# Kernel tuning notes

Hardware: AMD Instinct MI355X
Metric: run time of the kernel (lower is better)

Reference implementation:

```python
import jax, jax.numpy as jnp
import numpy as np

NTOKEN, NINP, NHID, NLAYERS = 32000, 1024, 1024, 2
SEQ, BATCH = 128, 32


def setup_inputs() -> dict:
    key = jax.random.key(0)
    ks = jax.random.split(key, 6)
    initrange = 0.1
    tokens = jax.random.randint(ks[0], (SEQ, BATCH), 0, NTOKEN)
    h0 = jnp.zeros((NLAYERS, BATCH, NHID), jnp.float32)
    c0 = jnp.zeros((NLAYERS, BATCH, NHID), jnp.float32)
    emb_table = jax.random.uniform(ks[1], (NTOKEN, NINP), jnp.float32, -initrange, initrange)
    # nn.Linear(2H, 4H): weight [4H, 2H]; store transposed [2H, 4H] for x @ W
    lstm_W = jax.random.normal(ks[2], (NLAYERS, 2 * NHID, 4 * NHID), jnp.float32) * (1.0 / np.sqrt(2 * NHID))
    lstm_b = jax.random.normal(ks[3], (NLAYERS, 4 * NHID), jnp.float32) * 0.01
    dec_W = jax.random.uniform(ks[4], (NHID, NTOKEN), jnp.float32, -initrange, initrange)
    dec_b = jnp.zeros((NTOKEN,), jnp.float32)
    return {"tokens": tokens, "h0": h0, "c0": c0, "emb_table": emb_table,
            "lstm_W": lstm_W, "lstm_b": lstm_b, "dec_W": dec_W, "dec_b": dec_b}


def _lstm_scan(emb, h0, c0, lstm_W, lstm_b):
    def step(carry, x_t):  # x_t: [B, H]
        h, c = carry  # each [L, B, H]
        hs, cs = [], []
        inp = x_t
        for l in range(NLAYERS):
            gates = jnp.concatenate([inp, h[l]], axis=1) @ lstm_W[l] + lstm_b[l]  # [B, 4H]
            i, j, f, o = jnp.split(gates, 4, axis=1)
            c_new = c[l] * jax.nn.sigmoid(f) + jax.nn.sigmoid(i) * jnp.tanh(j)
            h_new = jnp.tanh(c_new) * jax.nn.sigmoid(o)
            hs.append(h_new)
            cs.append(c_new)
            inp = h_new
        return (jnp.stack(hs), jnp.stack(cs)), inp

    (h_last, c_last), outputs = jax.lax.scan(step, (h0, c0), emb)
    return outputs, h_last, c_last  # outputs: [S, B, H]


def reference(tokens, h0, c0, emb_table, lstm_W, lstm_b, dec_W, dec_b):
    emb = emb_table[tokens]  # [S, B, NINP]
    outputs, h_last, c_last = _lstm_scan(emb, h0, c0, lstm_W, lstm_b)
    decoded = outputs @ dec_W + dec_b  # [S, B, NTOKEN]
    return decoded, (h_last, c_last)
```

## Files before the change

### kernel.cpp

```cpp
#include <hip/hip_runtime.h>

typedef __attribute__((ext_vector_type(8))) short bf16x8;
typedef __attribute__((ext_vector_type(4))) float f32x4;
typedef const __attribute__((address_space(1))) void* gas_ptr;
typedef __attribute__((address_space(3))) void* las_ptr;

__device__ __forceinline__ unsigned short f2bf(float f) {
  unsigned int u = __float_as_uint(f);
  return (unsigned short)((u + 0x7fffu + ((u >> 16) & 1u)) >> 16);
}
__device__ __forceinline__ unsigned int cvt_pk_bf16(float a, float b) {
  unsigned int r;
  asm volatile("v_cvt_pk_bf16_f32 %0, %1, %2" : "=v"(r) : "v"(a), "v"(b));
  return r;
}
__device__ __forceinline__ float sigm(float x) { return 1.0f / (1.0f + __expf(-x)); }

__device__ __forceinline__ void st_cv(unsigned int* p, unsigned int v) {
  __hip_atomic_store(p, v, __ATOMIC_RELAXED, __HIP_MEMORY_SCOPE_AGENT);
}

__device__ __forceinline__ void gbar_arrive(int* bars, int target, int bid) {
  int* leaf  = bars + (bid & 15) * 32;
  int* mcnt  = bars + 512;
  int* sense = bars + 640;
  if (__hip_atomic_fetch_add(leaf, 1, __ATOMIC_RELAXED, __HIP_MEMORY_SCOPE_AGENT) == 15) {
    __hip_atomic_store(leaf, 0, __ATOMIC_RELAXED, __HIP_MEMORY_SCOPE_AGENT);
    if (__hip_atomic_fetch_add(mcnt, 1, __ATOMIC_RELAXED, __HIP_MEMORY_SCOPE_AGENT) == 15) {
      __hip_atomic_store(mcnt, 0, __ATOMIC_RELAXED, __HIP_MEMORY_SCOPE_AGENT);
      __hip_atomic_store(sense, target, __ATOMIC_RELAXED, __HIP_MEMORY_SCOPE_AGENT);
    }
  }
}
__device__ __forceinline__ void gbar_wait(int* bars, int target) {
  int* sense = bars + 640;
  while (__hip_atomic_load(sense, __ATOMIC_RELAXED, __HIP_MEMORY_SCOPE_AGENT) < target)
    __builtin_amdgcn_s_sleep(1);
}

__global__ __launch_bounds__(256) void init_kernel(
    const float* __restrict__ h0_in,
    unsigned short* __restrict__ h0buf, unsigned short* __restrict__ h1buf,
    int* __restrict__ bar)
{
  const int j = blockIdx.x * 256 + threadIdx.x;
  if (j < 768) bar[j] = 0;
  h0buf[j] = f2bf(h0_in[j]);
  h1buf[32768 + j] = f2bf(h0_in[32768 + j]);
}

__global__ __launch_bounds__(256) void gather_emb(
    const int* __restrict__ tokens, const float* __restrict__ etab,
    unsigned short* __restrict__ xemb)
{
  const int r = blockIdx.x;
  const float* src = etab + (size_t)tokens[r] * 1024;
  const int q = threadIdx.x * 4;
  const float4 v = *(const float4*)(src + q);
  uint2 o;
  o.x = cvt_pk_bf16(v.x, v.y);
  o.y = cvt_pk_bf16(v.z, v.w);
  *(uint2*)(xemb + (size_t)r * 1024 + q) = o;
}

__global__ __launch_bounds__(256) void reorg_lstm_w(
    const float* __restrict__ W, char* __restrict__ wimg)
{
  __shared__ float tile[64 * 36];
  const int bid = blockIdx.x;
  const int layer = bid >> 7;
  const int u0 = (bid & 127) * 8;
  const int tid = threadIdx.x;
  const float* Wl = W + (size_t)layer * 2048 * 4096;
  char* img = wimg + (size_t)bid * 131072;
  const int kl = tid >> 2, g = tid & 3;
  const int row = tid & 15, ksub = (tid >> 4) & 3;
  const int tn = (tid >> 6) & 1, kl2 = tid >> 7;
  const int c = tn * 16 + row;
#pragma unroll 1
  for (int kt = 0; kt < 32; ++kt) {
    const float* src = Wl + (size_t)(kt * 64 + kl) * 4096 + g * 1024 + u0;
    const float4 v0 = *(const float4*)src;
    const float4 v1 = *(const float4*)(src + 4);
    *(float4*)(tile + kl * 36 + g * 8) = v0;
    *(float4*)(tile + kl * 36 + g * 8 + 4) = v1;
    __syncthreads();
    const int kbase = kl2 * 32 + ksub * 8;
    uint4 u;
    u.x = cvt_pk_bf16(tile[(kbase + 0) * 36 + c], tile[(kbase + 1) * 36 + c]);
    u.y = cvt_pk_bf16(tile[(kbase + 2) * 36 + c], tile[(kbase + 3) * 36 + c]);
    u.z = cvt_pk_bf16(tile[(kbase + 4) * 36 + c], tile[(kbase + 5) * 36 + c]);
    u.w = cvt_pk_bf16(tile[(kbase + 6) * 36 + c], tile[(kbase + 7) * 36 + c]);
    const int S = (kt * 2 + kl2) * 128 + tn * 64 + ksub * 16 + row;
    *(uint4*)(img + (size_t)S * 16) = u;
    __syncthreads();
  }
}

__global__ __launch_bounds__(512, 1) void lstm_seq_kernel(
    const char* __restrict__ wimg, const float* __restrict__ bias,
    const float* __restrict__ c0_in,
    const unsigned short* __restrict__ xemb,
    unsigned short* __restrict__ h0buf, unsigned short* __restrict__ h1buf,
    unsigned short* __restrict__ hseq,
    float* __restrict__ out_tail, int* __restrict__ bar)
{
  __shared__ __align__(16) char smem[148608];
  char* wlds   = smem;
  float* red   = (float*)(smem + 131072);
  float* gates = (float*)(smem + 143360);
  float* cl    = (float*)(smem + 147584);

  const int tid = threadIdx.x;
  const int bid = blockIdx.x;
  const int layer = bid >> 7;
  const int u0 = (bid & 127) * 8;
  const int lane = tid & 63, w = tid >> 6;
  const int tb = w & 1, kq = w >> 1;
  const int row = tb * 16 + (lane & 15);
  const int kg = lane >> 4;
  unsigned short* hmy = layer ? h1buf : h0buf;
  const bool statx = (layer == 0) && (kq < 2);

  {
    const char* img = wimg + (size_t)bid * 131072;
#pragma unroll 1
    for (int i = 0; i < 16; ++i) {
      const int off = (i * 512 + tid) * 16;
      __builtin_amdgcn_global_load_lds((gas_ptr)(img + off), (las_ptr)(wlds + off), 16, 0, 0);
    }
    if (tid < 256) cl[tid] = c0_in[layer * 32768 + (tid >> 3) * 1024 + u0 + (tid & 7)];
  }
  const int cc = lane & 15;
  const float biasv0 = bias[layer * 4096 + (cc >> 3) * 1024 + u0 + (cc & 7)];
  const float biasv1 = bias[layer * 4096 + ((cc + 16) >> 3) * 1024 + u0 + (cc & 7)];
  asm volatile("s_waitcnt vmcnt(0)");
  __syncthreads();

  const char* wq = wlds + (size_t)(kq * 16 * 128 + lane) * 16;

  bf16x8 a[16];
  if (statx) {
    const char* xn = (const char*)xemb + row * 2048 + kq * 1024 + kg * 16;
#pragma unroll
    for (int j = 0; j < 16; ++j) a[j] = *(const bf16x8*)(xn + j * 64);
  }

  for (int p = 0; p <= 128; ++p) {
    const bool active = layer ? (p >= 1) : (p < 128);
    if (active) {
      const int t = layer ? (p - 1) : p;
      f32x4 acc0 = {0.f, 0.f, 0.f, 0.f}, acc1 = {0.f, 0.f, 0.f, 0.f};

      if (!statx) {
        const char* src = (layer && kq < 2) ? (const char*)h0buf : (const char*)hmy;
        const char* xb = src + (p & 1) * 65536 + row * 2048 + (kq & 1) * 1024 + kg * 16;
#pragma unroll
        for (int j = 0; j < 16; ++j)
          asm volatile("global_load_dwordx4 %0, %1, off sc0 sc1"
                       : "=v"(a[j]) : "v"(xb + j * 64) : "memory");
        auto mm4 = [&](int j0) {
#pragma unroll
          for (int j = j0; j < j0 + 4; ++j) {
            const bf16x8 b0 = *(const bf16x8*)(wq + (size_t)j * 2048);
            const bf16x8 b1 = *(const bf16x8*)(wq + (size_t)j * 2048 + 1024);
            acc0 = __builtin_amdgcn_mfma_f32_16x16x32_bf16(a[j], b0, acc0, 0, 0, 0);
            acc1 = __builtin_amdgcn_mfma_f32_16x16x32_bf16(a[j], b1, acc1, 0, 0, 0);
          }
        };
        asm volatile("s_waitcnt vmcnt(12)" ::: "memory");
        __builtin_amdgcn_sched_barrier(0);
        mm4(0);
        asm volatile("s_waitcnt vmcnt(8)" ::: "memory");
        __builtin_amdgcn_sched_barrier(0);
        mm4(4);
        asm volatile("s_waitcnt vmcnt(4)" ::: "memory");
        __builtin_amdgcn_sched_barrier(0);
        mm4(8);
        asm volatile("s_waitcnt vmcnt(0)" ::: "memory");
        __builtin_amdgcn_sched_barrier(0);
        mm4(12);
      } else {
#pragma unroll
        for (int j = 0; j < 16; ++j) {
          const bf16x8 b0 = *(const bf16x8*)(wq + (size_t)j * 2048);
          const bf16x8 b1 = *(const bf16x8*)(wq + (size_t)j * 2048 + 1024);
          acc0 = __builtin_amdgcn_mfma_f32_16x16x32_bf16(a[j], b0, acc0, 0, 0, 0);
          acc1 = __builtin_amdgcn_mfma_f32_16x16x32_bf16(a[j], b1, acc1, 0, 0, 0);
        }
      }

      if (kq > 0) {
        const int s0 = (((kq - 1) * 2 + tb) * 2 + 0) * 64 + lane;
        const int s1 = (((kq - 1) * 2 + tb) * 2 + 1) * 64 + lane;
        *(f32x4*)(red + s0 * 4) = acc0;
        *(f32x4*)(red + s1 * 4) = acc1;
      }
      __syncthreads();
      if (kq == 0) {
#pragma unroll
        for (int q = 1; q < 4; ++q) {
          const f32x4 o0 = *(const f32x4*)(red + ((((q - 1) * 2 + tb) * 2 + 0) * 64 + lane) * 4);
          const f32x4 o1 = *(const f32x4*)(red + ((((q - 1) * 2 + tb) * 2 + 1) * 64 + lane) * 4);
#pragma unroll
          for (int r = 0; r < 4; ++r) { acc0[r] += o0[r]; acc1[r] += o1[r]; }
        }
        const int rb = tb * 16 + kg * 4;
#pragma unroll
        for (int r = 0; r < 4; ++r) {
          gates[(rb + r) * 33 + cc] = acc0[r] + biasv0;
          gates[(rb + r) * 33 + 16 + cc] = acc1[r] + biasv1;
        }
      }
      __syncthreads();
      if (tid < 128) {
        const int cb = tid >> 2, up = (tid & 3) * 2;
        const float gi0 = gates[cb * 33 + up],      gi1 = gates[cb * 33 + up + 1];
        const float gj0 = gates[cb * 33 + 8 + up],  gj1 = gates[cb * 33 + 9 + up];
        const float gf0 = gates[cb * 33 + 16 + up], gf1 = gates[cb * 33 + 17 + up];
        const float go0 = gates[cb * 33 + 24 + up], go1 = gates[cb * 33 + 25 + up];
        const float cn0 = cl[cb * 8 + up] * sigm(gf0) + sigm(gi0) * tanhf(gj0);
        const float cn1 = cl[cb * 8 + up + 1] * sigm(gf1) + sigm(gi1) * tanhf(gj1);
        const float hn0 = tanhf(cn0) * sigm(go0);
        const float hn1 = tanhf(cn1) * sigm(go1);
        cl[cb * 8 + up] = cn0;
        cl[cb * 8 + up + 1] = cn1;
        const unsigned int pk = cvt_pk_bf16(hn0, hn1);
        st_cv((unsigned int*)(hmy + ((p + 1) & 1) * 32768 + cb * 1024 + u0 + up), pk);
        if (layer) *(unsigned int*)(hseq + (size_t)t * 32768 + cb * 1024 + u0 + up) = pk;
        if (t == 127) {
          float* ot = out_tail + layer * 32768 + cb * 1024 + u0 + up;
          ot[0] = hn0; ot[1] = hn1;
          ot[65536] = cn0; ot[65537] = cn1;
        }
      }
    }

    if (p < 128) {
      __syncthreads();
      if (tid == 0) gbar_arrive(bar, p + 1, bid);
      if (statx && (p + 1) < 128) {
        const char* xn = (const char*)xemb + (size_t)(p + 1) * 65536 + row * 2048 + kq * 1024 + kg * 16;
#pragma unroll
        for (int j = 0; j < 16; ++j) a[j] = *(const bf16x8*)(xn + j * 64);
      }
      if (tid == 0) gbar_wait(bar, p + 1);
      __syncthreads();
    }
  }
}

__global__ __launch_bounds__(256) void transpose_decw_kernel(
    const float* __restrict__ decW, unsigned short* __restrict__ Wt)
{
  __shared__ float tile[64 * 68];
  const int bid = blockIdx.x;
  const int k0 = (bid & 15) * 64;
  const int n0 = (bid >> 4) * 64;
  const int tid = threadIdx.x;
  {
    const int kl = tid >> 4, c4 = (tid & 15) * 4;
#pragma unroll
    for (int i = 0; i < 4; ++i) {
      const int kr = kl + 16 * i;
      *(float4*)(tile + kr * 68 + c4) =
          *(const float4*)(decW + (size_t)(k0 + kr) * 32000 + n0 + c4);
    }
  }
  __syncthreads();
  {
    const int nl = tid >> 3, kc = (tid & 7) * 8;
#pragma unroll
    for (int h2 = 0; h2 < 2; ++h2) {
      const int n = nl + 32 * h2;
      float tv[8];
#pragma unroll
      for (int q = 0; q < 8; ++q) tv[q] = tile[(kc + q) * 68 + n];
      uint4 u;
      u.x = cvt_pk_bf16(tv[0], tv[1]);
      u.y = cvt_pk_bf16(tv[2], tv[3]);
      u.z = cvt_pk_bf16(tv[4], tv[5]);
      u.w = cvt_pk_bf16(tv[6], tv[7]);
      *(uint4*)(Wt + (size_t)(n0 + n) * 1024 + k0 + kc) = u;
    }
  }
}

__global__ __launch_bounds__(256) void decoder_kernel(
    const unsigned short* __restrict__ A,
    const unsigned short* __restrict__ Bt,
    const float* __restrict__ decb,
    float* __restrict__ out)
{
  __shared__ unsigned short Al[2][128 * 32];
  __shared__ unsigned short Bl[2][128 * 32];

  const int bid = blockIdx.x;
  const int swz = (bid & 7) * 1000 + (bid >> 3);
  const int mt = swz / 250, nt = swz % 250;
  const int m0 = mt * 128, n0 = nt * 128;

  const int tid = threadIdx.x;
  const int lane = tid & 63;
  const int wv = tid >> 6;
  const int wr = wv >> 1, wc = wv & 1;
  const int l15 = lane & 15, kg = lane >> 4;

  f32x4 acc[4][4];
#pragma unroll
  for (int mi = 0; mi < 4; ++mi)
#pragma unroll
    for (int ni = 0; ni < 4; ++ni) {
      f32x4 z = {0.f, 0.f, 0.f, 0.f};
      acc[mi][ni] = z;
    }

  auto stage = [&](const unsigned short* src, int row0, int k0, unsigned short* lds) {
#pragma unroll
    for (int j = 0; j < 2; ++j) {
      const int chunk = (wv * 2 + j) * 64 + lane;
      const int r = chunk >> 2, kc = chunk & 3;
      const unsigned short* g = src + (size_t)(row0 + r) * 1024 + k0 + kc * 8;
      __builtin_amdgcn_global_load_lds((gas_ptr)g, (las_ptr)(lds + chunk * 8), 16, 0, 0);
    }
  };

  stage(A, m0, 0, Al[0]);
  stage(Bt, n0, 0, Bl[0]);
  __syncthreads();

  int buf = 0;
  for (int kt = 0; kt < 32; ++kt) {
    if (kt < 31) {
      stage(A, m0, (kt + 1) * 32, Al[buf ^ 1]);
      stage(Bt, n0, (kt + 1) * 32, Bl[buf ^ 1]);
    }
    bf16x8 a[4], b[4];
#pragma unroll
    for (int mi = 0; mi < 4; ++mi)
      a[mi] = *(const bf16x8*)&Al[buf][(wr * 64 + mi * 16 + l15) * 32 + kg * 8];
#pragma unroll
    for (int ni = 0; ni < 4; ++ni)
      b[ni] = *(const bf16x8*)&Bl[buf][(wc * 64 + ni * 16 + l15) * 32 + kg * 8];
#pragma unroll
    for (int mi = 0; mi < 4; ++mi)
#pragma unroll
      for (int ni = 0; ni < 4; ++ni)
        acc[mi][ni] = __builtin_amdgcn_mfma_f32_16x16x32_bf16(a[mi], b[ni], acc[mi][ni], 0, 0, 0);
    __syncthreads();
    buf ^= 1;
  }

#pragma unroll
  for (int ni = 0; ni < 4; ++ni) {
    const int ocol = n0 + wc * 64 + ni * 16 + l15;
    const float bv = decb[ocol];
#pragma unroll
    for (int mi = 0; mi < 4; ++mi) {
      const int orow = m0 + wr * 64 + mi * 16 + kg * 4;
#pragma unroll
      for (int r = 0; r < 4; ++r)
        out[(size_t)(orow + r) * 32000 + ocol] = acc[mi][ni][r] + bv;
    }
  }
}

extern "C" void kernel_launch(void* const* d_in, const int* in_sizes, int n_in,
                              void* d_out, int out_size, void* d_ws, size_t ws_size,
                              hipStream_t stream) {
  (void)in_sizes; (void)n_in; (void)out_size; (void)ws_size;
  const int* tokens  = (const int*)d_in[0];
  const float* h0_in = (const float*)d_in[1];
  const float* c0_in = (const float*)d_in[2];
  const float* etab  = (const float*)d_in[3];
  const float* lstmW = (const float*)d_in[4];
  const float* lstmb = (const float*)d_in[5];
  const float* decW  = (const float*)d_in[6];
  const float* decb  = (const float*)d_in[7];
  float* out = (float*)d_out;

  char* ws = (char*)d_ws;
  unsigned short* hseq  = (unsigned short*)(ws + 0);
  char* img             = ws + 8388608;
  unsigned short* Wt    = (unsigned short*)(ws + 8388608);
  unsigned short* xemb  = (unsigned short*)(ws + 41943040);
  unsigned short* h0buf = (unsigned short*)(ws + 73924608);
  unsigned short* h1buf = (unsigned short*)(ws + 74055680);
  int* bar              = (int*)(ws + 74186752);

  init_kernel<<<128, 256, 0, stream>>>(h0_in, h0buf, h1buf, bar);
  gather_emb<<<4096, 256, 0, stream>>>(tokens, etab, xemb);
  reorg_lstm_w<<<256, 256, 0, stream>>>(lstmW, img);
  lstm_seq_kernel<<<256, 512, 0, stream>>>(img, lstmb, c0_in, xemb,
                                           h0buf, h1buf, hseq,
                                           out + 131072000, bar);
  transpose_decw_kernel<<<8000, 256, 0, stream>>>(decW, Wt);
  decoder_kernel<<<8000, 256, 0, stream>>>(hseq, Wt, decb, out);
}
```

Measured before the change: 1.362 ms.

## Enlarge decoder GEMM tiles to 256x256 with swizzled LDS and simplify grid barrier

The decoder GEMM moves from 128x128 tiles with 4 waves to 256x256 tiles with 8 waves. It uses K-steps of 64, an XOR-swizzled 128KB LDS double buffer, loads for the next step interleaved with the MFMAs, and s_setprio around the MFMA bursts. The aim is to cut global and LDS traffic per FLOP and avoid LDS bank conflicts, at the cost of one block per CU and higher register pressure. The LSTM grid barrier is also simplified to a monotonic counter that waiters compare against 16*target, which removes the sense-flag store from the critical path.

```diff
diff --git a/kernel.cpp b/kernel.cpp
--- a/kernel.cpp
+++ b/kernel.cpp
@@ -20,21 +20,18 @@
   __hip_atomic_store(p, v, __ATOMIC_RELAXED, __HIP_MEMORY_SCOPE_AGENT);
 }
 
-__device__ __forceinline__ void gbar_arrive(int* bars, int target, int bid) {
-  int* leaf  = bars + (bid & 15) * 32;
-  int* mcnt  = bars + 512;
-  int* sense = bars + 640;
+__device__ __forceinline__ void gbar_arrive(int* bars, int bid) {
+  int* leaf = bars + (bid & 15) * 32;
+  int* mcnt = bars + 512;
   if (__hip_atomic_fetch_add(leaf, 1, __ATOMIC_RELAXED, __HIP_MEMORY_SCOPE_AGENT) == 15) {
     __hip_atomic_store(leaf, 0, __ATOMIC_RELAXED, __HIP_MEMORY_SCOPE_AGENT);
-    if (__hip_atomic_fetch_add(mcnt, 1, __ATOMIC_RELAXED, __HIP_MEMORY_SCOPE_AGENT) == 15) {
-      __hip_atomic_store(mcnt, 0, __ATOMIC_RELAXED, __HIP_MEMORY_SCOPE_AGENT);
-      __hip_atomic_store(sense, target, __ATOMIC_RELAXED, __HIP_MEMORY_SCOPE_AGENT);
-    }
+    __hip_atomic_fetch_add(mcnt, 1, __ATOMIC_RELAXED, __HIP_MEMORY_SCOPE_AGENT);
   }
 }
 __device__ __forceinline__ void gbar_wait(int* bars, int target) {
-  int* sense = bars + 640;
-  while (__hip_atomic_load(sense, __ATOMIC_RELAXED, __HIP_MEMORY_SCOPE_AGENT) < target)
+  int* mcnt = bars + 512;
+  const int tgt = 16 * target;
+  while (__hip_atomic_load(mcnt, __ATOMIC_RELAXED, __HIP_MEMORY_SCOPE_AGENT) < tgt)
     __builtin_amdgcn_s_sleep(1);
 }
 
@@ -238,7 +235,7 @@
 
     if (p < 128) {
       __syncthreads();
-      if (tid == 0) gbar_arrive(bar, p + 1, bid);
+      if (tid == 0) gbar_arrive(bar, bid);
       if (statx && (p + 1) < 128) {
         const char* xn = (const char*)xemb + (size_t)(p + 1) * 65536 + row * 2048 + kq * 1024 + kg * 16;
 #pragma unroll
@@ -286,78 +283,95 @@
   }
 }
 
-__global__ __launch_bounds__(256) void decoder_kernel(
+__global__ __launch_bounds__(512, 1) void decoder_kernel(
     const unsigned short* __restrict__ A,
     const unsigned short* __restrict__ Bt,
     const float* __restrict__ decb,
     float* __restrict__ out)
 {
-  __shared__ unsigned short Al[2][128 * 32];
-  __shared__ unsigned short Bl[2][128 * 32];
+  __shared__ __align__(16) char lds[131072];
 
   const int bid = blockIdx.x;
-  const int swz = (bid & 7) * 1000 + (bid >> 3);
-  const int mt = swz / 250, nt = swz % 250;
-  const int m0 = mt * 128, n0 = nt * 128;
+  const int swz = (bid & 7) * 250 + (bid >> 3);
+  const int mt = swz / 125, nt = swz % 125;
+  const int m0 = mt * 256, n0 = nt * 256;
 
   const int tid = threadIdx.x;
   const int lane = tid & 63;
   const int wv = tid >> 6;
-  const int wr = wv >> 1, wc = wv & 1;
+  const int wm = wv >> 2, wn = wv & 3;
   const int l15 = lane & 15, kg = lane >> 4;
 
-  f32x4 acc[4][4];
-#pragma unroll
-  for (int mi = 0; mi < 4; ++mi)
+  f32x4 acc[8][4];
+#pragma unroll
+  for (int mi = 0; mi < 8; ++mi)
 #pragma unroll
     for (int ni = 0; ni < 4; ++ni) {
       f32x4 z = {0.f, 0.f, 0.f, 0.f};
       acc[mi][ni] = z;
     }
 
-  auto stage = [&](const unsigned short* src, int row0, int k0, unsigned short* lds) {
-#pragma unroll
-    for (int j = 0; j < 2; ++j) {
-      const int chunk = (wv * 2 + j) * 64 + lane;
-      const int r = chunk >> 2, kc = chunk & 3;
-      const unsigned short* g = src + (size_t)(row0 + r) * 1024 + k0 + kc * 8;
-      __builtin_amdgcn_global_load_lds((gas_ptr)g, (las_ptr)(lds + chunk * 8), 16, 0, 0);
+  auto stage4 = [&](int kt, int half) {
+    char* bufw = lds + (kt & 1) * 65536 + half * 32768;
+    const unsigned short* base = half ? Bt : A;
+    const int r0 = half ? n0 : m0;
+#pragma unroll
+    for (int j = 0; j < 4; ++j) {
+      const int o  = (j * 512 + tid) * 16;
+      const int os = o ^ (((o >> 9) & 1) << 5);
+      const int r  = os >> 7, kb = os & 127;
+      const unsigned short* g = base + (size_t)(r0 + r) * 1024 + kt * 64 + kb / 2;
+      __builtin_amdgcn_global_load_lds((gas_ptr)g, (las_ptr)(bufw + o), 16, 0, 0);
     }
   };
 
-  stage(A, m0, 0, Al[0]);
-  stage(Bt, n0, 0, Bl[0]);
+  stage4(0, 0);
+  stage4(0, 1);
   __syncthreads();
 
-  int buf = 0;
-  for (int kt = 0; kt < 32; ++kt) {
-    if (kt < 31) {
-      stage(A, m0, (kt + 1) * 32, Al[buf ^ 1]);
-      stage(Bt, n0, (kt + 1) * 32, Bl[buf ^ 1]);
-    }
-    bf16x8 a[4], b[4];
-#pragma unroll
-    for (int mi = 0; mi < 4; ++mi)
-      a[mi] = *(const bf16x8*)&Al[buf][(wr * 64 + mi * 16 + l15) * 32 + kg * 8];
-#pragma unroll
-    for (int ni = 0; ni < 4; ++ni)
-      b[ni] = *(const bf16x8*)&Bl[buf][(wc * 64 + ni * 16 + l15) * 32 + kg * 8];
-#pragma unroll
-    for (int mi = 0; mi < 4; ++mi)
-#pragma unroll
-      for (int ni = 0; ni < 4; ++ni)
-        acc[mi][ni] = __builtin_amdgcn_mfma_f32_16x16x32_bf16(a[mi], b[ni], acc[mi][ni], 0, 0, 0);
+  for (int kt = 0; kt < 16; ++kt) {
+    const char* bufr = lds + (kt & 1) * 65536;
+    bf16x8 bfr[4];
+#pragma unroll
+    for (int ks = 0; ks < 2; ++ks) {
+#pragma unroll
+      for (int mh = 0; mh < 2; ++mh) {
+        bf16x8 af[4];
+#pragma unroll
+        for (int q = 0; q < 4; ++q) {
+          const int r = wm * 128 + (mh * 4 + q) * 16 + l15;
+          const int o = (r * 128 + ks * 64 + kg * 16) ^ (((r >> 2) & 1) << 5);
+          af[q] = *(const bf16x8*)(bufr + o);
+        }
+        if (mh == 0) {
+#pragma unroll
+          for (int q = 0; q < 4; ++q) {
+            const int r = wn * 64 + q * 16 + l15;
+            const int o = (r * 128 + ks * 64 + kg * 16) ^ (((r >> 2) & 1) << 5);
+            bfr[q] = *(const bf16x8*)(bufr + 32768 + o);
+          }
+        }
+        if (ks == 0 && kt < 15) stage4(kt + 1, mh);
+        __builtin_amdgcn_s_setprio(1);
+#pragma unroll
+        for (int q = 0; q < 4; ++q)
+#pragma unroll
+          for (int ni = 0; ni < 4; ++ni)
+            acc[mh * 4 + q][ni] =
+                __builtin_amdgcn_mfma_f32_16x16x32_bf16(af[q], bfr[ni], acc[mh * 4 + q][ni], 0, 0, 0);
+        __builtin_amdgcn_s_setprio(0);
+      }
+    }
     __syncthreads();
-    buf ^= 1;
   }
 
 #pragma unroll
   for (int ni = 0; ni < 4; ++ni) {
-    const int ocol = n0 + wc * 64 + ni * 16 + l15;
+    const int ocol = n0 + wn * 64 + ni * 16 + l15;
     const float bv = decb[ocol];
 #pragma unroll
-    for (int mi = 0; mi < 4; ++mi) {
-      const int orow = m0 + wr * 64 + mi * 16 + kg * 4;
+    for (int mi = 0; mi < 8; ++mi) {
+      const int orow = m0 + wm * 128 + mi * 16 + kg * 4;
 #pragma unroll
       for (int r = 0; r < 4; ++r)
         out[(size_t)(orow + r) * 32000 + ocol] = acc[mi][ni][r] + bv;
@@ -395,5 +409,5 @@
                                            h0buf, h1buf, hseq,
                                            out + 131072000, bar);
   transpose_decw_kernel<<<8000, 256, 0, stream>>>(decW, Wt);
-  decoder_kernel<<<8000, 256, 0, stream>>>(hseq, Wt, decb, out);
-}
+  decoder_kernel<<<2000, 512, 0, stream>>>(hseq, Wt, decb, out);
+}
```

After: 1.408 ms. +3.4%, slower.
